# Performance work log

Measured on AMD Instinct MI355X. Metric: run time of the kernel, lower is better.

Reference implementation:

```python
import jax, jax.numpy as jnp
import numpy as np

D_MODEL = 2048
NUM_HEADS = 16
HEAD_DIM = D_MODEL // NUM_HEADS
BATCH = 2
SEQ = 2048


def setup_inputs() -> dict:
    key = jax.random.key(0)
    ks = jax.random.split(key, 5)
    scale = 1.0 / np.sqrt(D_MODEL)
    x = jax.random.normal(ks[0], (BATCH, SEQ, D_MODEL), dtype=jnp.float32)
    wq = jax.random.normal(ks[1], (D_MODEL, D_MODEL), dtype=jnp.float32) * scale
    wk = jax.random.normal(ks[2], (D_MODEL, D_MODEL), dtype=jnp.float32) * scale
    wv = jax.random.normal(ks[3], (D_MODEL, D_MODEL), dtype=jnp.float32) * scale
    wo = jax.random.normal(ks[4], (D_MODEL, D_MODEL), dtype=jnp.float32) * scale
    return {"x": x, "wq": wq, "wk": wk, "wv": wv, "wo": wo}


def reference(x, wq, wk, wv, wo):
    # x: [B, S, D_MODEL]; torch nn.Linear(bias=False): y = x @ W.T
    B, S, _ = x.shape

    def split_heads(t):
        # [B, S, D] -> [B, H, S, Dh]
        return t.reshape(B, S, NUM_HEADS, HEAD_DIM).transpose(0, 2, 1, 3)

    q = split_heads(x @ wq.T)
    k = split_heads(x @ wk.T)
    v = split_heads(x @ wv.T)

    # scaled dot-product attention with causal (tril) mask, single-rank path
    scores = jnp.einsum("bhqd,bhkd->bhqk", q, k) / jnp.sqrt(
        jnp.asarray(HEAD_DIM, dtype=x.dtype)
    )
    causal = jnp.tril(jnp.ones((S, S), dtype=bool))  # [S, S]
    neg_inf = jnp.asarray(jnp.finfo(scores.dtype).min, dtype=scores.dtype)
    scores = jnp.where(causal[None, None, :, :], scores, neg_inf)
    attn = jax.nn.softmax(scores, axis=-1)

    out = jnp.einsum("bhqk,bhkd->bhqd", attn, v)  # [B, H, S, Dh]
    out = out.transpose(0, 2, 1, 3).reshape(B, S, D_MODEL)
    return out @ wo.T
```

## Files before the change

### kernel.cpp

```cpp
#include <hip/hip_runtime.h>
#include <hip/hip_bf16.h>

#define D_MODEL   2048
#define NUM_HEADS 16
#define HEAD_DIM  128
#define BATCH     2
#define SEQ       2048

typedef short bf16x8 __attribute__((ext_vector_type(8)));
typedef float f32x4  __attribute__((ext_vector_type(4)));

__device__ inline short f2bf(float x) {
    __hip_bfloat16 h = __float2bfloat16(x);
    return *reinterpret_cast<short*>(&h);
}

__device__ inline void async_copy16(const void* g, void* l) {
    __builtin_amdgcn_global_load_lds(
        (const __attribute__((address_space(1))) void*)g,
        (__attribute__((address_space(3))) void*)l, 16, 0, 0);
}
__device__ inline void wait_all() { __builtin_amdgcn_s_waitcnt(0); }

__global__ __launch_bounds__(256) void f32_to_bf16(
    const float* __restrict__ src, __hip_bfloat16* __restrict__ dst, int n8) {
    const int i = blockIdx.x * 256 + threadIdx.x;
    if (i >= n8) return;
    const f32x4* p = (const f32x4*)src + (size_t)i * 2;
    f32x4 f0 = p[0], f1 = p[1];
    bf16x8 v;
#pragma unroll
    for (int j = 0; j < 4; ++j) { v[j] = f2bf(f0[j]); v[4 + j] = f2bf(f1[j]); }
    *(bf16x8*)((short*)dst + (size_t)i * 8) = v;
}

template <bool OUT_F32>
__global__ __launch_bounds__(256) void gemm_v3(
    const __hip_bfloat16* __restrict__ A,
    const __hip_bfloat16* __restrict__ W0,
    const __hip_bfloat16* __restrict__ W1,
    const __hip_bfloat16* __restrict__ W2,
    void* __restrict__ C0, void* __restrict__ C1, void* __restrict__ C2,
    int M, int N, int K) {
    __shared__ __hip_bfloat16 As[128 * 32];
    __shared__ __hip_bfloat16 Ws[128 * 32];

    const int z = blockIdx.z;
    const __hip_bfloat16* W = (z == 0) ? W0 : (z == 1) ? W1 : W2;
    void* Cv = (z == 0) ? C0 : (z == 1) ? C1 : C2;

    const int tid  = threadIdx.x;
    const int lane = tid & 63;
    const int wv   = tid >> 6;
    const int c    = lane & 15;
    const int quad = lane >> 4;
    const int m0   = blockIdx.y * 128;
    const int n0   = blockIdx.x * 128;
    const int wm   = (wv >> 1) * 64;
    const int wn   = (wv & 1) * 64;

    f32x4 acc[4][4];
#pragma unroll
    for (int mi = 0; mi < 4; ++mi)
#pragma unroll
        for (int ni = 0; ni < 4; ++ni)
            acc[mi][ni] = (f32x4){0.f, 0.f, 0.f, 0.f};

    const int nk = K >> 5;
    for (int kb = 0; kb < nk; ++kb) {
        __syncthreads();
#pragma unroll
        for (int i = 0; i < 2; ++i) {
            const int o   = wv * 2048 + i * 1024 + lane * 16;
            const int row = o >> 6;
            const int col = (o & 63) >> 1;
            async_copy16(&A[(size_t)(m0 + row) * K + kb * 32 + col], (char*)As + o);
            async_copy16(&W[(size_t)(n0 + row) * K + kb * 32 + col], (char*)Ws + o);
        }
        wait_all();
        __syncthreads();

        bf16x8 a[4], b[4];
#pragma unroll
        for (int mi = 0; mi < 4; ++mi)
            a[mi] = *(const bf16x8*)((const short*)As + (wm + mi * 16 + c) * 32 + quad * 8);
#pragma unroll
        for (int ni = 0; ni < 4; ++ni)
            b[ni] = *(const bf16x8*)((const short*)Ws + (wn + ni * 16 + c) * 32 + quad * 8);
#pragma unroll
        for (int mi = 0; mi < 4; ++mi)
#pragma unroll
            for (int ni = 0; ni < 4; ++ni)
                acc[mi][ni] = __builtin_amdgcn_mfma_f32_16x16x32_bf16(
                    a[mi], b[ni], acc[mi][ni], 0, 0, 0);
    }

#pragma unroll
    for (int mi = 0; mi < 4; ++mi)
#pragma unroll
        for (int ni = 0; ni < 4; ++ni)
#pragma unroll
            for (int r = 0; r < 4; ++r) {
                const int m = m0 + wm + mi * 16 + quad * 4 + r;
                const int n = n0 + wn + ni * 16 + c;
                if (OUT_F32)
                    ((float*)Cv)[(size_t)m * N + n] = acc[mi][ni][r];
                else
                    ((__hip_bfloat16*)Cv)[(size_t)m * N + n] = __float2bfloat16(acc[mi][ni][r]);
            }
}

__global__ __launch_bounds__(256) void transpose2k(
    const __hip_bfloat16* __restrict__ Vin, __hip_bfloat16* __restrict__ Vout) {
    __shared__ short T[64 * 72];
    const int tid = threadIdx.x;
    const int d0  = blockIdx.x * 64;
    const int s0  = blockIdx.y * 64;
    const size_t half = (size_t)SEQ * D_MODEL;
    const short* in  = (const short*)Vin + blockIdx.z * half;
    short*       out = (short*)Vout      + blockIdx.z * half;

#pragma unroll
    for (int i = 0; i < 2; ++i) {
        const int lin = i * 256 + tid;
        const int sr  = lin >> 3;
        const int sg  = lin & 7;
        *(uint4*)&T[sr * 72 + sg * 8] =
            *(const uint4*)&in[(size_t)(s0 + sr) * D_MODEL + d0 + sg * 8];
    }
    __syncthreads();
#pragma unroll
    for (int i = 0; i < 2; ++i) {
        const int lin = i * 256 + tid;
        const int dr  = lin >> 3;
        const int sg  = lin & 7;
        bf16x8 v;
#pragma unroll
        for (int j = 0; j < 8; ++j) v[j] = T[(sg * 8 + j) * 72 + dr];
        *(uint4*)&out[(size_t)(d0 + dr) * SEQ + s0 + sg * 8] = *(uint4*)&v;
    }
}

__global__ __launch_bounds__(256) void attn_v7(
    const __hip_bfloat16* Qg,
    const __hip_bfloat16* __restrict__ Kg,
    const __hip_bfloat16* __restrict__ Vt,
    __hip_bfloat16* Og) {
    constexpr int LDP = 72;
    __shared__ short Ks[2][64 * 128];
    __shared__ short Vs[2][128 * 64];
    __shared__ __hip_bfloat16 Pl[64 * LDP];
    __shared__ float l_l[64];

    const int tid  = threadIdx.x;
    const int lane = tid & 63;
    const int w    = tid >> 6;
    const int c    = lane & 15;
    const int quad = lane >> 4;
    const int qlo  = blockIdx.x;
    const int qhi  = (SEQ / 64 - 1) - qlo;
    const int h    = blockIdx.y;
    const size_t half = (size_t)SEQ * D_MODEL;
    const __hip_bfloat16* Qb  = Qg + blockIdx.z * half;
    const __hip_bfloat16* Kb  = Kg + blockIdx.z * half;
    const __hip_bfloat16* Vtb = Vt + blockIdx.z * half;
    __hip_bfloat16*       Ob  = Og + blockIdx.z * half;
    const size_t base = (size_t)h * HEAD_DIM;
    const int dt0 = w * 2;
    const float scale = 0.08838834764831845f;

    for (int pass = 0; pass < 2; ++pass) {
        const int myq = pass ? qlo : qhi;
        const int q0  = myq * 64;
        const int wq0 = q0 + w * 16;

        bf16x8 qf[4];
#pragma unroll
        for (int kk = 0; kk < 4; ++kk)
            qf[kk] = *(const bf16x8*)((const short*)Qb + base +
                                      (size_t)(wq0 + c) * D_MODEL + kk * 32 + quad * 8);

        float l_run[4] = {0.f, 0.f, 0.f, 0.f};
        f32x4 o_acc[4][2];
#pragma unroll
        for (int qt = 0; qt < 4; ++qt)
#pragma unroll
            for (int dd = 0; dd < 2; ++dd)
                o_acc[qt][dd] = (f32x4){0.f, 0.f, 0.f, 0.f};

#pragma unroll
        for (int i = 0; i < 4; ++i) {
            const int o = (i * 256 + tid) * 16;
            {
                const int row = o >> 8, colb = o & 255;
                const int scol = colb ^ ((row & 7) << 4);
                async_copy16((const char*)(Kb + base + (size_t)row * D_MODEL) + scol,
                             (char*)Ks[0] + o);
            }
            {
                const int row = o >> 7, colb = o & 127;
                const int scol = colb ^ ((row & 7) << 4);
                async_copy16((const char*)(Vtb + (size_t)(base + row) * SEQ) + scol,
                             (char*)Vs[0] + o);
            }
        }
        wait_all();
        __syncthreads();

        int cur = 0;
        const int nch = myq + 1;
        for (int ch = 0; ch < nch; ++ch) {
            if (ch + 1 < nch) {
                const int key0n = (ch + 1) * 64;
#pragma unroll
                for (int i = 0; i < 4; ++i) {
                    const int o = (i * 256 + tid) * 16;
                    {
                        const int row = o >> 8, colb = o & 255;
                        const int scol = colb ^ ((row & 7) << 4);
                        async_copy16((const char*)(Kb + base + (size_t)(key0n + row) * D_MODEL) + scol,
                                     (char*)Ks[cur ^ 1] + o);
                    }
                    {
                        const int row = o >> 7, colb = o & 127;
                        const int scol = colb ^ ((row & 7) << 4);
                        async_copy16((const char*)(Vtb + (size_t)(base + row) * SEQ + key0n) + scol,
                                     (char*)Vs[cur ^ 1] + o);
                    }
                }
            }

            const int key0 = ch * 64;
            const short* Ksc = Ks[cur];
            const short* Vsc = Vs[cur];
            f32x4 s[4];
#pragma unroll
            for (int kt = 0; kt < 4; ++kt) s[kt] = (f32x4){0.f, 0.f, 0.f, 0.f};
            __builtin_amdgcn_s_setprio(1);
#pragma unroll
            for (int kk = 0; kk < 4; ++kk)
#pragma unroll
                for (int kt = 0; kt < 4; ++kt) {
                    const int r  = kt * 16 + c;
                    const int cb = (kk * 64 + quad * 16) ^ ((r & 7) << 4);
                    bf16x8 kf = *(const bf16x8*)((const char*)Ksc + r * 256 + cb);
                    s[kt] = __builtin_amdgcn_mfma_f32_16x16x32_bf16(qf[kk], kf, s[kt], 0, 0, 0);
                }
            __builtin_amdgcn_s_setprio(0);

            const bool diag = (ch == myq);
#pragma unroll
            for (int r = 0; r < 4; ++r) {
                const int qg = wq0 + quad * 4 + r;
                const int lrow = w * 16 + quad * 4 + r;
                float p[4], rs = 0.f;
#pragma unroll
                for (int kt = 0; kt < 4; ++kt) {
                    float v = s[kt][r] * scale;
                    if (diag && (key0 + kt * 16 + c > qg)) v = -1e30f;
                    p[kt] = __expf(v);
                    rs += p[kt];
                }
#pragma unroll
                for (int off = 1; off < 16; off <<= 1)
                    rs += __shfl_xor(rs, off);
                l_run[r] += rs;
#pragma unroll
                for (int kt = 0; kt < 4; ++kt)
                    Pl[lrow * LDP + kt * 16 + c] = __float2bfloat16(p[kt]);
            }
            __syncthreads();

#pragma unroll
            for (int kk = 0; kk < 2; ++kk) {
                bf16x8 pa[4];
#pragma unroll
                for (int qt = 0; qt < 4; ++qt)
                    pa[qt] = *(const bf16x8*)((const short*)Pl +
                                              (qt * 16 + c) * LDP + kk * 32 + quad * 8);
                __builtin_amdgcn_s_setprio(1);
#pragma unroll
                for (int dd = 0; dd < 2; ++dd) {
                    const int rv  = (dt0 + dd) * 16 + c;
                    const int cbv = (kk * 64 + quad * 16) ^ ((rv & 7) << 4);
                    bf16x8 vb = *(const bf16x8*)((const char*)Vsc + rv * 128 + cbv);
#pragma unroll
                    for (int qt = 0; qt < 4; ++qt)
                        o_acc[qt][dd] = __builtin_amdgcn_mfma_f32_16x16x32_bf16(
                            pa[qt], vb, o_acc[qt][dd], 0, 0, 0);
                }
                __builtin_amdgcn_s_setprio(0);
            }

            __syncthreads();
            cur ^= 1;
        }

        if (c == 0)
#pragma unroll
            for (int r = 0; r < 4; ++r) l_l[w * 16 + quad * 4 + r] = l_run[r];
        __syncthreads();

#pragma unroll
        for (int qt = 0; qt < 4; ++qt)
#pragma unroll
            for (int r = 0; r < 4; ++r) {
                const float inv = 1.0f / l_l[qt * 16 + quad * 4 + r];
                const int row = q0 + qt * 16 + quad * 4 + r;
#pragma unroll
                for (int dd = 0; dd < 2; ++dd)
                    Ob[base + (size_t)row * D_MODEL + (dt0 + dd) * 16 + c] =
                        __float2bfloat16(o_acc[qt][dd][r] * inv);
            }
        __syncthreads();
    }
}

template <bool A_F32, bool W_F32, bool OUT_F32>
__global__ __launch_bounds__(256) void gemm_bt(
    const void* __restrict__ Av, const void* __restrict__ Wv,
    void* __restrict__ Cv, int M, int N, int K) {
    __shared__ __hip_bfloat16 As[128 * 32];
    __shared__ __hip_bfloat16 Ws[128 * 32];
    const int tid = threadIdx.x, lane = tid & 63, wv = tid >> 6;
    const int c = lane & 15, quad = lane >> 4;
    const int m0 = blockIdx.y * 128, n0 = blockIdx.x * 128;
    const int wm = (wv >> 1) * 64, wn = (wv & 1) * 64;
    f32x4 acc[4][4];
#pragma unroll
    for (int mi = 0; mi < 4; ++mi)
#pragma unroll
        for (int ni = 0; ni < 4; ++ni) acc[mi][ni] = (f32x4){0.f, 0.f, 0.f, 0.f};
    const int nk = K >> 5;
    for (int kb = 0; kb < nk; ++kb) {
        __syncthreads();
#pragma unroll
        for (int i = 0; i < 2; ++i) {
            const int e = (i * 256 + tid) * 8;
            const int row = e >> 5, col = e & 31;
            if (A_F32) {
                const float* p = (const float*)Av + (size_t)(m0 + row) * K + kb * 32 + col;
                f32x4 f0 = *(const f32x4*)p, f1 = *(const f32x4*)(p + 4);
                bf16x8 v;
#pragma unroll
                for (int j = 0; j < 4; ++j) { v[j] = f2bf(f0[j]); v[4 + j] = f2bf(f1[j]); }
                *(bf16x8*)((short*)As + e) = v;
            } else {
                *(uint4*)((short*)As + e) =
                    *(const uint4*)((const short*)Av + (size_t)(m0 + row) * K + kb * 32 + col);
            }
            if (W_F32) {
                const float* p = (const float*)Wv + (size_t)(n0 + row) * K + kb * 32 + col;
                f32x4 f0 = *(const f32x4*)p, f1 = *(const f32x4*)(p + 4);
                bf16x8 v;
#pragma unroll
                for (int j = 0; j < 4; ++j) { v[j] = f2bf(f0[j]); v[4 + j] = f2bf(f1[j]); }
                *(bf16x8*)((short*)Ws + e) = v;
            } else {
                *(uint4*)((short*)Ws + e) =
                    *(const uint4*)((const short*)Wv + (size_t)(n0 + row) * K + kb * 32 + col);
            }
        }
        __syncthreads();
        bf16x8 a[4], b[4];
#pragma unroll
        for (int mi = 0; mi < 4; ++mi)
            a[mi] = *(const bf16x8*)((const short*)As + (wm + mi * 16 + c) * 32 + quad * 8);
#pragma unroll
        for (int ni = 0; ni < 4; ++ni)
            b[ni] = *(const bf16x8*)((const short*)Ws + (wn + ni * 16 + c) * 32 + quad * 8);
#pragma unroll
        for (int mi = 0; mi < 4; ++mi)
#pragma unroll
            for (int ni = 0; ni < 4; ++ni)
                acc[mi][ni] = __builtin_amdgcn_mfma_f32_16x16x32_bf16(a[mi], b[ni], acc[mi][ni], 0, 0, 0);
    }
#pragma unroll
    for (int mi = 0; mi < 4; ++mi)
#pragma unroll
        for (int ni = 0; ni < 4; ++ni)
#pragma unroll
            for (int r = 0; r < 4; ++r) {
                const int m = m0 + wm + mi * 16 + quad * 4 + r;
                const int n = n0 + wn + ni * 16 + c;
                if (OUT_F32) ((float*)Cv)[(size_t)m * N + n] = acc[mi][ni][r];
                else ((__hip_bfloat16*)Cv)[(size_t)m * N + n] = __float2bfloat16(acc[mi][ni][r]);
            }
}

__global__ __launch_bounds__(256) void attn_fused_v2(
    const __hip_bfloat16* Qg, const __hip_bfloat16* __restrict__ Kg,
    const __hip_bfloat16* __restrict__ Vg, __hip_bfloat16* Og) {
    constexpr int LDK = 136, LDP = 72;
    __shared__ __hip_bfloat16 Kc[64 * LDK];
    __shared__ __hip_bfloat16 Vc[64 * LDK];
    __shared__ __hip_bfloat16 Pl[64 * LDP];
    __shared__ float alpha_l[64];
    __shared__ float l_l[64];
    const int tid = threadIdx.x, lane = tid & 63, w = tid >> 6;
    const int c = lane & 15, quad = lane >> 4;
    const int qb = blockIdx.x, h = blockIdx.y;
    const size_t base = (size_t)h * HEAD_DIM;
    const int q0 = qb * 64, wq0 = q0 + w * 16, dt0 = w * 2;
    bf16x8 qf[4];
#pragma unroll
    for (int kk = 0; kk < 4; ++kk)
        qf[kk] = *(const bf16x8*)((const short*)Qg + base +
                                  (size_t)(wq0 + c) * D_MODEL + kk * 32 + quad * 8);
    float m_run[4], l_run[4];
#pragma unroll
    for (int r = 0; r < 4; ++r) { m_run[r] = -1e30f; l_run[r] = 0.f; }
    f32x4 o_acc[4][2];
#pragma unroll
    for (int qt = 0; qt < 4; ++qt)
#pragma unroll
        for (int dd = 0; dd < 2; ++dd) o_acc[qt][dd] = (f32x4){0.f, 0.f, 0.f, 0.f};
    const float scale = 0.08838834764831845f;
    const int nch = qb + 1;
    for (int ch = 0; ch < nch; ++ch) {
        const int key0 = ch * 64;
        __syncthreads();
#pragma unroll
        for (int i = 0; i < 4; ++i) {
            const int lin = i * 256 + tid;
            const int kr = lin >> 4, cg = lin & 15;
            *(uint4*)((short*)Kc + kr * LDK + cg * 8) =
                *(const uint4*)&Kg[base + (size_t)(key0 + kr) * D_MODEL + cg * 8];
            *(uint4*)((short*)Vc + kr * LDK + cg * 8) =
                *(const uint4*)&Vg[base + (size_t)(key0 + kr) * D_MODEL + cg * 8];
        }
        __syncthreads();
        f32x4 s[4];
#pragma unroll
        for (int kt = 0; kt < 4; ++kt) s[kt] = (f32x4){0.f, 0.f, 0.f, 0.f};
#pragma unroll
        for (int kk = 0; kk < 4; ++kk)
#pragma unroll
            for (int kt = 0; kt < 4; ++kt) {
                bf16x8 kb = *(const bf16x8*)((const short*)Kc + (kt * 16 + c) * LDK + kk * 32 + quad * 8);
                s[kt] = __builtin_amdgcn_mfma_f32_16x16x32_bf16(qf[kk], kb, s[kt], 0, 0, 0);
            }
#pragma unroll
        for (int r = 0; r < 4; ++r) {
            const int qg = wq0 + quad * 4 + r;
            float v[4];
#pragma unroll
            for (int kt = 0; kt < 4; ++kt) {
                v[kt] = s[kt][r] * scale;
                if (key0 + kt * 16 + c > qg) v[kt] = -1e30f;
            }
            float mx = fmaxf(fmaxf(v[0], v[1]), fmaxf(v[2], v[3]));
#pragma unroll
            for (int off = 1; off < 16; off <<= 1) mx = fmaxf(mx, __shfl_xor(mx, off));
            const float m_new = fmaxf(m_run[r], mx);
            const float al = __expf(m_run[r] - m_new);
            float p[4], rs = 0.f;
#pragma unroll
            for (int kt = 0; kt < 4; ++kt) { p[kt] = __expf(v[kt] - m_new); rs += p[kt]; }
#pragma unroll
            for (int off = 1; off < 16; off <<= 1) rs += __shfl_xor(rs, off);
            l_run[r] = l_run[r] * al + rs;
            m_run[r] = m_new;
            const int lrow = w * 16 + quad * 4 + r;
#pragma unroll
            for (int kt = 0; kt < 4; ++kt) Pl[lrow * LDP + kt * 16 + c] = __float2bfloat16(p[kt]);
            if (c == 0) alpha_l[lrow] = al;
        }
        __syncthreads();
#pragma unroll
        for (int qt = 0; qt < 4; ++qt)
#pragma unroll
            for (int r = 0; r < 4; ++r) {
                const float al = alpha_l[qt * 16 + quad * 4 + r];
                o_acc[qt][0][r] *= al;
                o_acc[qt][1][r] *= al;
            }
#pragma unroll
        for (int kk = 0; kk < 2; ++kk) {
            bf16x8 pa[4];
#pragma unroll
            for (int qt = 0; qt < 4; ++qt)
                pa[qt] = *(const bf16x8*)((const short*)Pl + (qt * 16 + c) * LDP + kk * 32 + quad * 8);
#pragma unroll
            for (int dd = 0; dd < 2; ++dd) {
                bf16x8 vb;
#pragma unroll
                for (int j = 0; j < 8; ++j)
                    vb[j] = ((const short*)Vc)[(kk * 32 + quad * 8 + j) * LDK + (dt0 + dd) * 16 + c];
#pragma unroll
                for (int qt = 0; qt < 4; ++qt)
                    o_acc[qt][dd] = __builtin_amdgcn_mfma_f32_16x16x32_bf16(pa[qt], vb, o_acc[qt][dd], 0, 0, 0);
            }
        }
    }
    if (c == 0)
#pragma unroll
        for (int r = 0; r < 4; ++r) l_l[w * 16 + quad * 4 + r] = l_run[r];
    __syncthreads();
#pragma unroll
    for (int qt = 0; qt < 4; ++qt)
#pragma unroll
        for (int r = 0; r < 4; ++r) {
            const float inv = 1.0f / l_l[qt * 16 + quad * 4 + r];
            const int row = q0 + qt * 16 + quad * 4 + r;
#pragma unroll
            for (int dd = 0; dd < 2; ++dd)
                Og[base + (size_t)row * D_MODEL + (dt0 + dd) * 16 + c] =
                    __float2bfloat16(o_acc[qt][dd][r] * inv);
        }
}

extern "C" void kernel_launch(void* const* d_in, const int* in_sizes, int n_in,
                              void* d_out, int out_size, void* d_ws, size_t ws_size,
                              hipStream_t stream) {
    const float* x  = (const float*)d_in[0];
    const float* wq = (const float*)d_in[1];
    const float* wk = (const float*)d_in[2];
    const float* wv = (const float*)d_in[3];
    const float* wo = (const float*)d_in[4];
    float* out = (float*)d_out;

    const size_t half  = (size_t)SEQ * D_MODEL;
    const size_t WELEM = (size_t)D_MODEL * D_MODEL;
    const size_t needA = (4 * WELEM + 5 * 2 * half) * 2;
    const size_t needB = (4 * WELEM + 4 * half) * 2;

    if (ws_size >= needA) {
        __hip_bfloat16* wqb = (__hip_bfloat16*)d_ws;
        __hip_bfloat16* wkb = wqb + WELEM;
        __hip_bfloat16* wvb = wkb + WELEM;
        __hip_bfloat16* wob = wvb + WELEM;
        __hip_bfloat16* xb  = wob + WELEM;
        __hip_bfloat16* Q   = xb + 2 * half;
        __hip_bfloat16* Kf  = Q  + 2 * half;
        __hip_bfloat16* Vf  = Kf + 2 * half;
        __hip_bfloat16* Vt  = xb;

        f32_to_bf16<<<4096, 256, 0, stream>>>(x,  xb,  (int)(2 * half / 8));
        f32_to_bf16<<<2048, 256, 0, stream>>>(wq, wqb, (int)(WELEM / 8));
        f32_to_bf16<<<2048, 256, 0, stream>>>(wk, wkb, (int)(WELEM / 8));
        f32_to_bf16<<<2048, 256, 0, stream>>>(wv, wvb, (int)(WELEM / 8));
        f32_to_bf16<<<2048, 256, 0, stream>>>(wo, wob, (int)(WELEM / 8));

        gemm_v3<false><<<dim3(16, 32, 3), 256, 0, stream>>>(
            xb, wqb, wkb, wvb, Q, Kf, Vf, 4096, D_MODEL, D_MODEL);
        transpose2k<<<dim3(32, 32, 2), 256, 0, stream>>>(Vf, Vt);
        attn_v7<<<dim3(16, 16, 2), 256, 0, stream>>>(Q, Kf, Vt, Q);
        gemm_v3<true><<<dim3(16, 32, 1), 256, 0, stream>>>(
            Q, wob, wob, wob, out, out, out, 4096, D_MODEL, D_MODEL);
    } else if (ws_size >= needB) {
        __hip_bfloat16* wqb = (__hip_bfloat16*)d_ws;
        __hip_bfloat16* wkb = wqb + WELEM;
        __hip_bfloat16* wvb = wkb + WELEM;
        __hip_bfloat16* wob = wvb + WELEM;
        __hip_bfloat16* xbb = wob + WELEM;
        __hip_bfloat16* Qb  = xbb + half;
        __hip_bfloat16* Kb  = Qb + half;
        __hip_bfloat16* Vb  = Kb + half;
        __hip_bfloat16* Vtb = xbb;

        f32_to_bf16<<<2048, 256, 0, stream>>>(wq, wqb, (int)(WELEM / 8));
        f32_to_bf16<<<2048, 256, 0, stream>>>(wk, wkb, (int)(WELEM / 8));
        f32_to_bf16<<<2048, 256, 0, stream>>>(wv, wvb, (int)(WELEM / 8));
        f32_to_bf16<<<2048, 256, 0, stream>>>(wo, wob, (int)(WELEM / 8));
        for (int b = 0; b < BATCH; ++b) {
            f32_to_bf16<<<2048, 256, 0, stream>>>(x + b * half, xbb, (int)(half / 8));
            gemm_v3<false><<<dim3(16, 16, 3), 256, 0, stream>>>(
                xbb, wqb, wkb, wvb, Qb, Kb, Vb, 2048, D_MODEL, D_MODEL);
            transpose2k<<<dim3(32, 32, 1), 256, 0, stream>>>(Vb, Vtb);
            attn_v7<<<dim3(16, 16, 1), 256, 0, stream>>>(Qb, Kb, Vtb, Qb);
            gemm_v3<true><<<dim3(16, 16, 1), 256, 0, stream>>>(
                Qb, wob, wob, wob, out + b * half, out, out, 2048, D_MODEL, D_MODEL);
        }
    } else {
        __hip_bfloat16* Qb = (__hip_bfloat16*)d_ws;
        __hip_bfloat16* Kb = Qb + half;
        __hip_bfloat16* Vb = Kb + half;
        dim3 gg(16, 16);
        dim3 ga(32, 16);
        for (int b = 0; b < BATCH; ++b) {
            const float* xbp = x + b * half;
            gemm_bt<true, true, false><<<gg, 256, 0, stream>>>(xbp, wq, Qb, 2048, D_MODEL, D_MODEL);
            gemm_bt<true, true, false><<<gg, 256, 0, stream>>>(xbp, wk, Kb, 2048, D_MODEL, D_MODEL);
            gemm_bt<true, true, false><<<gg, 256, 0, stream>>>(xbp, wv, Vb, 2048, D_MODEL, D_MODEL);
            attn_fused_v2<<<ga, 256, 0, stream>>>(Qb, Kb, Vb, Qb);
            gemm_bt<false, true, true><<<gg, 256, 0, stream>>>(Qb, wo, out + b * half, 2048, D_MODEL, D_MODEL);
        }
    }
}
```

Measured before the change: 426.4 us.

## Give each attention wave its own rows for PV and fuse conversion launches

The attention kernel now has each wave own its 16 query rows across all 128 head dims in the P·V product. Each wave reads only the P tile it wrote itself, so the shared row-sum buffer and several block-wide barriers per chunk and per pass go away, and normalisation uses the per-wave running sums directly. The trade-off is more LDS reads of V fragments per wave (8 per kk instead of 2) and 8 accumulators per lane. Separately, the five fp32-to-bf16 conversion launches are merged into one kernel that picks its tensor from the block index, cutting launch overhead.

```diff
diff --git a/kernel.cpp b/kernel.cpp
--- a/kernel.cpp
+++ b/kernel.cpp
@@ -32,6 +32,28 @@
 #pragma unroll
     for (int j = 0; j < 4; ++j) { v[j] = f2bf(f0[j]); v[4 + j] = f2bf(f1[j]); }
     *(bf16x8*)((short*)dst + (size_t)i * 8) = v;
+}
+
+__global__ __launch_bounds__(256) void cvt5(
+    const float* __restrict__ x,  __hip_bfloat16* __restrict__ xb,
+    const float* __restrict__ w0, __hip_bfloat16* __restrict__ w0b,
+    const float* __restrict__ w1, __hip_bfloat16* __restrict__ w1b,
+    const float* __restrict__ w2, __hip_bfloat16* __restrict__ w2b,
+    const float* __restrict__ w3, __hip_bfloat16* __restrict__ w3b) {
+    const int b = blockIdx.x;
+    const float* src; short* dst; int idx;
+    if (b < 4096)       { src = x;  dst = (short*)xb;  idx = b; }
+    else if (b < 6144)  { src = w0; dst = (short*)w0b; idx = b - 4096; }
+    else if (b < 8192)  { src = w1; dst = (short*)w1b; idx = b - 6144; }
+    else if (b < 10240) { src = w2; dst = (short*)w2b; idx = b - 8192; }
+    else                { src = w3; dst = (short*)w3b; idx = b - 10240; }
+    const int i = idx * 256 + threadIdx.x;
+    const f32x4* p = (const f32x4*)src + (size_t)i * 2;
+    f32x4 f0 = p[0], f1 = p[1];
+    bf16x8 v;
+#pragma unroll
+    for (int j = 0; j < 4; ++j) { v[j] = f2bf(f0[j]); v[4 + j] = f2bf(f1[j]); }
+    *(bf16x8*)(dst + (size_t)i * 8) = v;
 }
 
 template <bool OUT_F32>
@@ -141,7 +163,7 @@
     }
 }
 
-__global__ __launch_bounds__(256) void attn_v7(
+__global__ __launch_bounds__(256) void attn_v8(
     const __hip_bfloat16* Qg,
     const __hip_bfloat16* __restrict__ Kg,
     const __hip_bfloat16* __restrict__ Vt,
@@ -150,7 +172,6 @@
     __shared__ short Ks[2][64 * 128];
     __shared__ short Vs[2][128 * 64];
     __shared__ __hip_bfloat16 Pl[64 * LDP];
-    __shared__ float l_l[64];
 
     const int tid  = threadIdx.x;
     const int lane = tid & 63;
@@ -166,13 +187,15 @@
     const __hip_bfloat16* Vtb = Vt + blockIdx.z * half;
     __hip_bfloat16*       Ob  = Og + blockIdx.z * half;
     const size_t base = (size_t)h * HEAD_DIM;
-    const int dt0 = w * 2;
+    const int prow0 = w * 16;
     const float scale = 0.08838834764831845f;
 
     for (int pass = 0; pass < 2; ++pass) {
         const int myq = pass ? qlo : qhi;
         const int q0  = myq * 64;
-        const int wq0 = q0 + w * 16;
+        const int wq0 = q0 + prow0;
+
+        __syncthreads();
 
         bf16x8 qf[4];
 #pragma unroll
@@ -181,12 +204,9 @@
                                       (size_t)(wq0 + c) * D_MODEL + kk * 32 + quad * 8);
 
         float l_run[4] = {0.f, 0.f, 0.f, 0.f};
-        f32x4 o_acc[4][2];
-#pragma unroll
-        for (int qt = 0; qt < 4; ++qt)
-#pragma unroll
-            for (int dd = 0; dd < 2; ++dd)
-                o_acc[qt][dd] = (f32x4){0.f, 0.f, 0.f, 0.f};
+        f32x4 o_acc[8];
+#pragma unroll
+        for (int dt = 0; dt < 8; ++dt) o_acc[dt] = (f32x4){0.f, 0.f, 0.f, 0.f};
 
 #pragma unroll
         for (int i = 0; i < 4; ++i) {
@@ -204,12 +224,12 @@
                              (char*)Vs[0] + o);
             }
         }
-        wait_all();
-        __syncthreads();
 
         int cur = 0;
         const int nch = myq + 1;
         for (int ch = 0; ch < nch; ++ch) {
+            __syncthreads();
+
             if (ch + 1 < nch) {
                 const int key0n = (ch + 1) * 64;
 #pragma unroll
@@ -252,7 +272,7 @@
 #pragma unroll
             for (int r = 0; r < 4; ++r) {
                 const int qg = wq0 + quad * 4 + r;
-                const int lrow = w * 16 + quad * 4 + r;
+                const int lrow = prow0 + quad * 4 + r;
                 float p[4], rs = 0.f;
 #pragma unroll
                 for (int kt = 0; kt < 4; ++kt) {
@@ -269,50 +289,34 @@
                 for (int kt = 0; kt < 4; ++kt)
                     Pl[lrow * LDP + kt * 16 + c] = __float2bfloat16(p[kt]);
             }
-            __syncthreads();
 
 #pragma unroll
             for (int kk = 0; kk < 2; ++kk) {
-                bf16x8 pa[4];
-#pragma unroll
-                for (int qt = 0; qt < 4; ++qt)
-                    pa[qt] = *(const bf16x8*)((const short*)Pl +
-                                              (qt * 16 + c) * LDP + kk * 32 + quad * 8);
+                bf16x8 pa = *(const bf16x8*)((const short*)Pl +
+                                             (prow0 + c) * LDP + kk * 32 + quad * 8);
                 __builtin_amdgcn_s_setprio(1);
 #pragma unroll
-                for (int dd = 0; dd < 2; ++dd) {
-                    const int rv  = (dt0 + dd) * 16 + c;
+                for (int dt = 0; dt < 8; ++dt) {
+                    const int rv  = dt * 16 + c;
                     const int cbv = (kk * 64 + quad * 16) ^ ((rv & 7) << 4);
                     bf16x8 vb = *(const bf16x8*)((const char*)Vsc + rv * 128 + cbv);
-#pragma unroll
-                    for (int qt = 0; qt < 4; ++qt)
-                        o_acc[qt][dd] = __builtin_amdgcn_mfma_f32_16x16x32_bf16(
-                            pa[qt], vb, o_acc[qt][dd], 0, 0, 0);
+                    o_acc[dt] = __builtin_amdgcn_mfma_f32_16x16x32_bf16(pa, vb, o_acc[dt], 0, 0, 0);
                 }
                 __builtin_amdgcn_s_setprio(0);
             }
 
-            __syncthreads();
             cur ^= 1;
         }
 
-        if (c == 0)
-#pragma unroll
-            for (int r = 0; r < 4; ++r) l_l[w * 16 + quad * 4 + r] = l_run[r];
-        __syncthreads();
-
-#pragma unroll
-        for (int qt = 0; qt < 4; ++qt)
-#pragma unroll
-            for (int r = 0; r < 4; ++r) {
-                const float inv = 1.0f / l_l[qt * 16 + quad * 4 + r];
-                const int row = q0 + qt * 16 + quad * 4 + r;
-#pragma unroll
-                for (int dd = 0; dd < 2; ++dd)
-                    Ob[base + (size_t)row * D_MODEL + (dt0 + dd) * 16 + c] =
-                        __float2bfloat16(o_acc[qt][dd][r] * inv);
-            }
-        __syncthreads();
+#pragma unroll
+        for (int r = 0; r < 4; ++r) {
+            const float inv = 1.0f / l_run[r];
+            const int row = wq0 + quad * 4 + r;
+#pragma unroll
+            for (int dt = 0; dt < 8; ++dt)
+                Ob[base + (size_t)row * D_MODEL + dt * 16 + c] =
+                    __float2bfloat16(o_acc[dt][r] * inv);
+        }
     }
 }
 
@@ -536,16 +540,12 @@
         __hip_bfloat16* Vf  = Kf + 2 * half;
         __hip_bfloat16* Vt  = xb;
 
-        f32_to_bf16<<<4096, 256, 0, stream>>>(x,  xb,  (int)(2 * half / 8));
-        f32_to_bf16<<<2048, 256, 0, stream>>>(wq, wqb, (int)(WELEM / 8));
-        f32_to_bf16<<<2048, 256, 0, stream>>>(wk, wkb, (int)(WELEM / 8));
-        f32_to_bf16<<<2048, 256, 0, stream>>>(wv, wvb, (int)(WELEM / 8));
-        f32_to_bf16<<<2048, 256, 0, stream>>>(wo, wob, (int)(WELEM / 8));
+        cvt5<<<12288, 256, 0, stream>>>(x, xb, wq, wqb, wk, wkb, wv, wvb, wo, wob);
 
         gemm_v3<false><<<dim3(16, 32, 3), 256, 0, stream>>>(
             xb, wqb, wkb, wvb, Q, Kf, Vf, 4096, D_MODEL, D_MODEL);
         transpose2k<<<dim3(32, 32, 2), 256, 0, stream>>>(Vf, Vt);
-        attn_v7<<<dim3(16, 16, 2), 256, 0, stream>>>(Q, Kf, Vt, Q);
+        attn_v8<<<dim3(16, 16, 2), 256, 0, stream>>>(Q, Kf, Vt, Q);
         gemm_v3<true><<<dim3(16, 32, 1), 256, 0, stream>>>(
             Q, wob, wob, wob, out, out, out, 4096, D_MODEL, D_MODEL);
     } else if (ws_size >= needB) {
@@ -568,7 +568,7 @@
             gemm_v3<false><<<dim3(16, 16, 3), 256, 0, stream>>>(
                 xbb, wqb, wkb, wvb, Qb, Kb, Vb, 2048, D_MODEL, D_MODEL);
             transpose2k<<<dim3(32, 32, 1), 256, 0, stream>>>(Vb, Vtb);
-            attn_v7<<<dim3(16, 16, 1), 256, 0, stream>>>(Qb, Kb, Vtb, Qb);
+            attn_v8<<<dim3(16, 16, 1), 256, 0, stream>>>(Qb, Kb, Vtb, Qb);
             gemm_v3<true><<<dim3(16, 16, 1), 256, 0, stream>>>(
                 Qb, wob, wob, wob, out + b * half, out, out, 2048, D_MODEL, D_MODEL);
         }
```

Result: no change. 423.7 us (-0.6%).
